# Optimization experiments

Hardware: AMD Instinct MI355X
Metric: run time of the kernel (lower is better)

The kernel has to match this reference:

```python
import jax, jax.numpy as jnp
import numpy as np

TOPK = 10
STEP = 0.1


def setup_inputs() -> dict:
    key = jax.random.key(0)
    k1, k2 = jax.random.split(key)
    N, C = 8192, 32768
    inp = jax.random.normal(k1, (N, C), dtype=jnp.float32)
    target = jax.random.normal(k2, (N,), dtype=jnp.float32)
    return {"input": inp, "target": target}


def reference(input, target):
    # topk over last dim: values [N, K], indices [N, K]
    values, index = jax.lax.top_k(input, TOPK)
    # Original: diag(value @ (index*step + 1).T) == row-wise dot product
    # pred[n] = sum_k values[n,k] * (index[n,k]*step + 1.0)
    weights = index.astype(values.dtype) * STEP + 1.0
    pred = jnp.sum(values * weights, axis=-1)  # [N]
    return jnp.mean(jnp.square(target - pred))
```

## Files before the change

### kernel.cpp

```cpp
#include <hip/hip_runtime.h>
#include <math.h>

#define N_ROWS 8192
#define N_COLS 32768
#define K_TOP 10
#define STEP_W 0.1f
#define THREADS 256
#define CAP 512
#define T0 3.0f
#define QPT 32
#define BATCH 8
#define OUTER (QPT / BATCH)

typedef float f4 __attribute__((ext_vector_type(4)));

#define TRY_INSERT(v, i)                                                      \
  do {                                                                        \
    if ((v) > tv[K_TOP - 1]) {                                                \
      tv[K_TOP - 1] = (v);                                                    \
      ti[K_TOP - 1] = (i);                                                    \
      _Pragma("unroll") for (int _j = K_TOP - 1; _j >= 1; --_j) {             \
        if (tv[_j] > tv[_j - 1]) {                                            \
          float _tv = tv[_j]; tv[_j] = tv[_j - 1]; tv[_j - 1] = _tv;          \
          int   _ti = ti[_j]; ti[_j] = ti[_j - 1]; ti[_j - 1] = _ti;          \
        }                                                                     \
      }                                                                       \
    }                                                                         \
  } while (0)

#define TRY_INSERT_TB(v, i)                                                   \
  do {                                                                        \
    if ((v) > tv[K_TOP - 1] ||                                                \
        ((v) == tv[K_TOP - 1] && (i) < ti[K_TOP - 1])) {                      \
      tv[K_TOP - 1] = (v);                                                    \
      ti[K_TOP - 1] = (i);                                                    \
      _Pragma("unroll") for (int _j = K_TOP - 1; _j >= 1; --_j) {             \
        if (tv[_j] > tv[_j - 1] ||                                            \
            (tv[_j] == tv[_j - 1] && ti[_j] < ti[_j - 1])) {                  \
          float _tv = tv[_j]; tv[_j] = tv[_j - 1]; tv[_j - 1] = _tv;          \
          int   _ti = ti[_j]; ti[_j] = ti[_j - 1]; ti[_j - 1] = _ti;          \
        }                                                                     \
      }                                                                       \
    }                                                                         \
  } while (0)

__global__ __launch_bounds__(THREADS) void filter_kernel(
    const float* __restrict__ inp, float* __restrict__ cand_v,
    int* __restrict__ cand_i, unsigned* __restrict__ cand_cnt) {
  __shared__ float lv[CAP];
  __shared__ int li[CAP];
  __shared__ unsigned cnt;

  const int row = blockIdx.x;
  const int tid = threadIdx.x;
  if (tid == 0) cnt = 0;
  __syncthreads();

  const f4* rp4 = reinterpret_cast<const f4*>(inp + (size_t)row * N_COLS);

  for (int it = 0; it < OUTER; ++it) {
    f4 d[BATCH];
#pragma unroll
    for (int j = 0; j < BATCH; ++j)
      d[j] = __builtin_nontemporal_load(&rp4[(it * BATCH + j) * THREADS + tid]);
#pragma unroll
    for (int j = 0; j < BATCH; ++j) {
      const int c0 = ((it * BATCH + j) * THREADS + tid) * 4;
      const float m = fmaxf(fmaxf(d[j][0], d[j][1]), fmaxf(d[j][2], d[j][3]));
      if (m >= T0) {
        if (d[j][0] >= T0) {
          const unsigned p = atomicAdd(&cnt, 1u);
          if (p < CAP) { lv[p] = d[j][0]; li[p] = c0 + 0; }
        }
        if (d[j][1] >= T0) {
          const unsigned p = atomicAdd(&cnt, 1u);
          if (p < CAP) { lv[p] = d[j][1]; li[p] = c0 + 1; }
        }
        if (d[j][2] >= T0) {
          const unsigned p = atomicAdd(&cnt, 1u);
          if (p < CAP) { lv[p] = d[j][2]; li[p] = c0 + 2; }
        }
        if (d[j][3] >= T0) {
          const unsigned p = atomicAdd(&cnt, 1u);
          if (p < CAP) { lv[p] = d[j][3]; li[p] = c0 + 3; }
        }
      }
    }
  }
  __syncthreads();

  const unsigned total = cnt;
  const unsigned stored = total < CAP ? total : CAP;
  float* dv = cand_v + (size_t)row * CAP;
  int* di = cand_i + (size_t)row * CAP;
  for (unsigned p = tid; p < stored; p += THREADS) {
    dv[p] = lv[p];
    di[p] = li[p];
  }
  if (tid == 0) cand_cnt[row] = total;
}

__global__ __launch_bounds__(THREADS) void select_kernel(
    const float* __restrict__ inp, const float* __restrict__ target,
    const float* __restrict__ cand_v, const int* __restrict__ cand_i,
    const unsigned* __restrict__ cand_cnt, float* __restrict__ row_err) {
  const int tid = threadIdx.x;
  const int lane = tid & 63;
  const int wid = tid >> 6;
  const int row = blockIdx.x * (THREADS / 64) + wid;

  float tv[K_TOP];
  int ti[K_TOP];
#pragma unroll
  for (int j = 0; j < K_TOP; ++j) {
    tv[j] = -INFINITY;
    ti[j] = 0x7FFFFFFF;
  }

  const unsigned total = cand_cnt[row];
  if (total >= K_TOP && total <= CAP) {
    const float* dv = cand_v + (size_t)row * CAP;
    const int* di = cand_i + (size_t)row * CAP;
    for (unsigned p = lane; p < total; p += 64) {
      const float v = dv[p];
      const int i = di[p];
      TRY_INSERT_TB(v, i);
    }
  } else {
    const float4* rp4 =
        reinterpret_cast<const float4*>(inp + (size_t)row * N_COLS);
#pragma unroll 8
    for (int it = 0; it < N_COLS / 4 / 64; ++it) {
      const int v4 = it * 64 + lane;
      const float4 d = rp4[v4];
      const int c0 = v4 * 4;
      const float m = fmaxf(fmaxf(d.x, d.y), fmaxf(d.z, d.w));
      if (m > tv[K_TOP - 1]) {
        TRY_INSERT(d.x, c0 + 0);
        TRY_INSERT(d.y, c0 + 1);
        TRY_INSERT(d.z, c0 + 2);
        TRY_INSERT(d.w, c0 + 3);
      }
    }
  }

  float pred = 0.0f;
#pragma unroll
  for (int k = 0; k < K_TOP; ++k) {
    float v = tv[0];
    int i = ti[0];
#pragma unroll
    for (int off = 32; off >= 1; off >>= 1) {
      const float ov = __shfl_xor(v, off, 64);
      const int oi = __shfl_xor(i, off, 64);
      if (ov > v || (ov == v && oi < i)) {
        v = ov;
        i = oi;
      }
    }
    pred += v * ((float)i * STEP_W + 1.0f);
    if (tv[0] == v && ti[0] == i) {
#pragma unroll
      for (int j = 0; j < K_TOP - 1; ++j) {
        tv[j] = tv[j + 1];
        ti[j] = ti[j + 1];
      }
      tv[K_TOP - 1] = -INFINITY;
      ti[K_TOP - 1] = 0x7FFFFFFF;
    }
  }

  if (lane == 0) {
    const float e = target[row] - pred;
    row_err[row] = e * e;
  }
}

__global__ __launch_bounds__(THREADS) void reduce_mean_kernel(
    const float* __restrict__ row_err, float* __restrict__ out) {
  const int tid = threadIdx.x;
  float s = 0.0f;
#pragma unroll
  for (int i = tid; i < N_ROWS; i += THREADS) s += row_err[i];
#pragma unroll
  for (int off = 32; off >= 1; off >>= 1) s += __shfl_xor(s, off, 64);
  __shared__ float sw[THREADS / 64];
  const int lane = tid & 63;
  const int wid = tid >> 6;
  if (lane == 0) sw[wid] = s;
  __syncthreads();
  if (tid == 0) {
    float t = 0.0f;
#pragma unroll
    for (int w = 0; w < THREADS / 64; ++w) t += sw[w];
    out[0] = t / (float)N_ROWS;
  }
}

extern "C" void kernel_launch(void* const* d_in, const int* in_sizes, int n_in,
                              void* d_out, int out_size, void* d_ws,
                              size_t ws_size, hipStream_t stream) {
  const float* inp = (const float*)d_in[0];
  const float* target = (const float*)d_in[1];
  float* out = (float*)d_out;

  char* ws = (char*)d_ws;
  float* row_err = (float*)ws;
  unsigned* cand_cnt = (unsigned*)(ws + 32 * 1024);
  float* cand_v = (float*)(ws + 64 * 1024);
  int* cand_i = (int*)(ws + 64 * 1024 + (size_t)N_ROWS * CAP * 4);

  filter_kernel<<<N_ROWS, THREADS, 0, stream>>>(inp, cand_v, cand_i, cand_cnt);
  select_kernel<<<N_ROWS / (THREADS / 64), THREADS, 0, stream>>>(
      inp, target, cand_v, cand_i, cand_cnt, row_err);
  reduce_mean_kernel<<<1, THREADS, 0, stream>>>(row_err, out);
}
```

Measured before the change: 195.2 us.

## Fuse filter and select kernels into one per-row top-k kernel

Merges the threshold filter and the candidate top-k selection into a single kernel, so candidates stay in shared memory instead of being written to and reread from global workspace. This removes one kernel launch and the global candidate traffic. The fallback path now scans the row with the whole block and merges per-wave maxima through shared memory with barriers. The final selection runs on only one wave while the other three sit idle.

```diff
diff --git a/kernel.cpp b/kernel.cpp
--- a/kernel.cpp
+++ b/kernel.cpp
@@ -44,106 +44,8 @@
     }                                                                         \
   } while (0)
 
-__global__ __launch_bounds__(THREADS) void filter_kernel(
-    const float* __restrict__ inp, float* __restrict__ cand_v,
-    int* __restrict__ cand_i, unsigned* __restrict__ cand_cnt) {
-  __shared__ float lv[CAP];
-  __shared__ int li[CAP];
-  __shared__ unsigned cnt;
-
-  const int row = blockIdx.x;
-  const int tid = threadIdx.x;
-  if (tid == 0) cnt = 0;
-  __syncthreads();
-
-  const f4* rp4 = reinterpret_cast<const f4*>(inp + (size_t)row * N_COLS);
-
-  for (int it = 0; it < OUTER; ++it) {
-    f4 d[BATCH];
-#pragma unroll
-    for (int j = 0; j < BATCH; ++j)
-      d[j] = __builtin_nontemporal_load(&rp4[(it * BATCH + j) * THREADS + tid]);
-#pragma unroll
-    for (int j = 0; j < BATCH; ++j) {
-      const int c0 = ((it * BATCH + j) * THREADS + tid) * 4;
-      const float m = fmaxf(fmaxf(d[j][0], d[j][1]), fmaxf(d[j][2], d[j][3]));
-      if (m >= T0) {
-        if (d[j][0] >= T0) {
-          const unsigned p = atomicAdd(&cnt, 1u);
-          if (p < CAP) { lv[p] = d[j][0]; li[p] = c0 + 0; }
-        }
-        if (d[j][1] >= T0) {
-          const unsigned p = atomicAdd(&cnt, 1u);
-          if (p < CAP) { lv[p] = d[j][1]; li[p] = c0 + 1; }
-        }
-        if (d[j][2] >= T0) {
-          const unsigned p = atomicAdd(&cnt, 1u);
-          if (p < CAP) { lv[p] = d[j][2]; li[p] = c0 + 2; }
-        }
-        if (d[j][3] >= T0) {
-          const unsigned p = atomicAdd(&cnt, 1u);
-          if (p < CAP) { lv[p] = d[j][3]; li[p] = c0 + 3; }
-        }
-      }
-    }
-  }
-  __syncthreads();
-
-  const unsigned total = cnt;
-  const unsigned stored = total < CAP ? total : CAP;
-  float* dv = cand_v + (size_t)row * CAP;
-  int* di = cand_i + (size_t)row * CAP;
-  for (unsigned p = tid; p < stored; p += THREADS) {
-    dv[p] = lv[p];
-    di[p] = li[p];
-  }
-  if (tid == 0) cand_cnt[row] = total;
-}
-
-__global__ __launch_bounds__(THREADS) void select_kernel(
-    const float* __restrict__ inp, const float* __restrict__ target,
-    const float* __restrict__ cand_v, const int* __restrict__ cand_i,
-    const unsigned* __restrict__ cand_cnt, float* __restrict__ row_err) {
-  const int tid = threadIdx.x;
-  const int lane = tid & 63;
-  const int wid = tid >> 6;
-  const int row = blockIdx.x * (THREADS / 64) + wid;
-
-  float tv[K_TOP];
-  int ti[K_TOP];
-#pragma unroll
-  for (int j = 0; j < K_TOP; ++j) {
-    tv[j] = -INFINITY;
-    ti[j] = 0x7FFFFFFF;
-  }
-
-  const unsigned total = cand_cnt[row];
-  if (total >= K_TOP && total <= CAP) {
-    const float* dv = cand_v + (size_t)row * CAP;
-    const int* di = cand_i + (size_t)row * CAP;
-    for (unsigned p = lane; p < total; p += 64) {
-      const float v = dv[p];
-      const int i = di[p];
-      TRY_INSERT_TB(v, i);
-    }
-  } else {
-    const float4* rp4 =
-        reinterpret_cast<const float4*>(inp + (size_t)row * N_COLS);
-#pragma unroll 8
-    for (int it = 0; it < N_COLS / 4 / 64; ++it) {
-      const int v4 = it * 64 + lane;
-      const float4 d = rp4[v4];
-      const int c0 = v4 * 4;
-      const float m = fmaxf(fmaxf(d.x, d.y), fmaxf(d.z, d.w));
-      if (m > tv[K_TOP - 1]) {
-        TRY_INSERT(d.x, c0 + 0);
-        TRY_INSERT(d.y, c0 + 1);
-        TRY_INSERT(d.z, c0 + 2);
-        TRY_INSERT(d.w, c0 + 3);
-      }
-    }
-  }
-
+__device__ __forceinline__ float wave_extract(float (&tv)[K_TOP],
+                                              int (&ti)[K_TOP]) {
   float pred = 0.0f;
 #pragma unroll
   for (int k = 0; k < K_TOP; ++k) {
@@ -169,10 +71,146 @@
       ti[K_TOP - 1] = 0x7FFFFFFF;
     }
   }
-
-  if (lane == 0) {
-    const float e = target[row] - pred;
-    row_err[row] = e * e;
+  return pred;
+}
+
+__global__ __launch_bounds__(THREADS) void fused_topk_kernel(
+    const float* __restrict__ inp, const float* __restrict__ target,
+    float* __restrict__ row_err) {
+  __shared__ float lv[CAP];
+  __shared__ int li[CAP];
+  __shared__ unsigned cnt;
+  __shared__ float sv[THREADS / 64];
+  __shared__ int si[THREADS / 64];
+
+  const int row = blockIdx.x;
+  const int tid = threadIdx.x;
+  const int lane = tid & 63;
+  const int wid = tid >> 6;
+  if (tid == 0) cnt = 0;
+  __syncthreads();
+
+  const f4* rp4 = reinterpret_cast<const f4*>(inp + (size_t)row * N_COLS);
+
+  for (int it = 0; it < OUTER; ++it) {
+    f4 d[BATCH];
+#pragma unroll
+    for (int j = 0; j < BATCH; ++j)
+      d[j] = __builtin_nontemporal_load(&rp4[(it * BATCH + j) * THREADS + tid]);
+#pragma unroll
+    for (int j = 0; j < BATCH; ++j) {
+      const int c0 = ((it * BATCH + j) * THREADS + tid) * 4;
+      const float m = fmaxf(fmaxf(d[j][0], d[j][1]), fmaxf(d[j][2], d[j][3]));
+      if (m >= T0) {
+        if (d[j][0] >= T0) {
+          const unsigned p = atomicAdd(&cnt, 1u);
+          if (p < CAP) { lv[p] = d[j][0]; li[p] = c0 + 0; }
+        }
+        if (d[j][1] >= T0) {
+          const unsigned p = atomicAdd(&cnt, 1u);
+          if (p < CAP) { lv[p] = d[j][1]; li[p] = c0 + 1; }
+        }
+        if (d[j][2] >= T0) {
+          const unsigned p = atomicAdd(&cnt, 1u);
+          if (p < CAP) { lv[p] = d[j][2]; li[p] = c0 + 2; }
+        }
+        if (d[j][3] >= T0) {
+          const unsigned p = atomicAdd(&cnt, 1u);
+          if (p < CAP) { lv[p] = d[j][3]; li[p] = c0 + 3; }
+        }
+      }
+    }
+  }
+  __syncthreads();
+  const unsigned total = cnt;
+
+  if (total >= K_TOP && total <= CAP) {
+    if (wid == 0) {
+      float tv[K_TOP];
+      int ti[K_TOP];
+#pragma unroll
+      for (int j = 0; j < K_TOP; ++j) {
+        tv[j] = -INFINITY;
+        ti[j] = 0x7FFFFFFF;
+      }
+      for (unsigned p = lane; p < total; p += 64) {
+        const float v = lv[p];
+        const int i = li[p];
+        TRY_INSERT_TB(v, i);
+      }
+      const float pred = wave_extract(tv, ti);
+      if (lane == 0) {
+        const float e = target[row] - pred;
+        row_err[row] = e * e;
+      }
+    }
+  } else {
+    float tv[K_TOP];
+    int ti[K_TOP];
+#pragma unroll
+    for (int j = 0; j < K_TOP; ++j) {
+      tv[j] = -INFINITY;
+      ti[j] = 0x7FFFFFFF;
+    }
+#pragma unroll 4
+    for (int it = 0; it < QPT; ++it) {
+      const int v4 = it * THREADS + tid;
+      const f4 d = rp4[v4];
+      const int c0 = v4 * 4;
+      const float m = fmaxf(fmaxf(d[0], d[1]), fmaxf(d[2], d[3]));
+      if (m > tv[K_TOP - 1]) {
+        TRY_INSERT(d[0], c0 + 0);
+        TRY_INSERT(d[1], c0 + 1);
+        TRY_INSERT(d[2], c0 + 2);
+        TRY_INSERT(d[3], c0 + 3);
+      }
+    }
+    float pred = 0.0f;
+#pragma unroll
+    for (int k = 0; k < K_TOP; ++k) {
+      float v = tv[0];
+      int i = ti[0];
+#pragma unroll
+      for (int off = 32; off >= 1; off >>= 1) {
+        const float ov = __shfl_xor(v, off, 64);
+        const int oi = __shfl_xor(i, off, 64);
+        if (ov > v || (ov == v && oi < i)) {
+          v = ov;
+          i = oi;
+        }
+      }
+      if (lane == 0) {
+        sv[wid] = v;
+        si[wid] = i;
+      }
+      __syncthreads();
+      float wv = sv[0];
+      int wi = si[0];
+#pragma unroll
+      for (int w = 1; w < THREADS / 64; ++w) {
+        const float ov = sv[w];
+        const int oi = si[w];
+        if (ov > wv || (ov == wv && oi < wi)) {
+          wv = ov;
+          wi = oi;
+        }
+      }
+      __syncthreads();
+      pred += wv * ((float)wi * STEP_W + 1.0f);
+      if (tv[0] == wv && ti[0] == wi) {
+#pragma unroll
+        for (int j = 0; j < K_TOP - 1; ++j) {
+          tv[j] = tv[j + 1];
+          ti[j] = ti[j + 1];
+        }
+        tv[K_TOP - 1] = -INFINITY;
+        ti[K_TOP - 1] = 0x7FFFFFFF;
+      }
+    }
+    if (tid == 0) {
+      const float e = target[row] - pred;
+      row_err[row] = e * e;
+    }
   }
 }
 
@@ -203,15 +241,8 @@
   const float* inp = (const float*)d_in[0];
   const float* target = (const float*)d_in[1];
   float* out = (float*)d_out;
-
-  char* ws = (char*)d_ws;
-  float* row_err = (float*)ws;
-  unsigned* cand_cnt = (unsigned*)(ws + 32 * 1024);
-  float* cand_v = (float*)(ws + 64 * 1024);
-  int* cand_i = (int*)(ws + 64 * 1024 + (size_t)N_ROWS * CAP * 4);
-
-  filter_kernel<<<N_ROWS, THREADS, 0, stream>>>(inp, cand_v, cand_i, cand_cnt);
-  select_kernel<<<N_ROWS / (THREADS / 64), THREADS, 0, stream>>>(
-      inp, target, cand_v, cand_i, cand_cnt, row_err);
+  float* row_err = (float*)d_ws;
+
+  fused_topk_kernel<<<N_ROWS, THREADS, 0, stream>>>(inp, target, row_err);
   reduce_mean_kernel<<<1, THREADS, 0, stream>>>(row_err, out);
 }
```

Result: faster. 174.1 us (-10.8%).
